# Performance work log

Hardware: AMD Instinct MI355X
Metric: run time of the kernel (lower is better)

Reference implementation:

```python
import jax, jax.numpy as jnp
import numpy as np

B, S, WIN5, E, H = 64, 2048, 50, 128, 256


def setup_inputs() -> dict:
    key = jax.random.key(0)
    ks = jax.random.split(key, 11)
    return {
        "prev_window": jax.random.normal(ks[0], (B, S, WIN5), dtype=jnp.float32),
        "W_emb": jax.random.normal(ks[1], (E, WIN5), dtype=jnp.float32) * 0.1,
        "b_emb": jax.random.normal(ks[2], (E,), dtype=jnp.float32) * 0.1,
        "W_ih": jax.random.normal(ks[3], (4 * H, E), dtype=jnp.float32) * 0.05,
        "W_hh": jax.random.normal(ks[4], (4 * H, H), dtype=jnp.float32) * 0.05,
        "b_ih": jax.random.normal(ks[5], (4 * H,), dtype=jnp.float32) * 0.05,
        "b_hh": jax.random.normal(ks[6], (4 * H,), dtype=jnp.float32) * 0.05,
        "W_out": jax.random.normal(ks[7], (1, H), dtype=jnp.float32) * 0.1,
        "b_out": jax.random.normal(ks[8], (1,), dtype=jnp.float32) * 0.1,
        "h0": jax.random.uniform(ks[9], (B, H), dtype=jnp.float32),
        "c0": jax.random.uniform(ks[10], (B, H), dtype=jnp.float32),
    }


def reference(prev_window, W_emb, b_emb, W_ih, W_hh, b_ih, b_hh, W_out, b_out, h0, c0):
    # embedding: [B, S, E], relu(Linear)
    emb = jax.nn.relu(jnp.einsum("bsw,ew->bse", prev_window, W_emb) + b_emb)
    # precompute input projections for all steps: [S, B, 4H]
    x_gates = jnp.einsum("bse,ge->sbg", emb, W_ih) + b_ih + b_hh

    def step(carry, xg):
        h, c = carry
        gates = xg + h @ W_hh.T  # [B, 4H]
        i, f, g, o = jnp.split(gates, 4, axis=-1)
        i = jax.nn.sigmoid(i)
        f = jax.nn.sigmoid(f)
        g = jnp.tanh(g)
        o = jax.nn.sigmoid(o)
        c = f * c + i * g
        h = o * jnp.tanh(c)
        return (h, c), h

    _, hs = jax.lax.scan(step, (h0, c0), x_gates)  # hs: [S, B, H]
    # dropout rate is 0.0 -> identity
    y = jax.nn.sigmoid(jnp.einsum("sbh,oh->sbo", hs, W_out) + b_out)  # [S, B, 1]
    return y
```

## Files before the change

### kernel.cpp

```cpp
#include <hip/hip_runtime.h>
#include <hip/hip_bf16.h>

#define B_ 64
#define S_ 2048
#define W_ 50
#define E_ 128
#define H_ 256
#define G_ 1024

typedef unsigned short u16;
typedef unsigned int u32;
typedef unsigned char u8;
typedef unsigned int v4u __attribute__((ext_vector_type(4)));
typedef __attribute__((ext_vector_type(8))) short short8;
typedef __attribute__((ext_vector_type(4))) float f32x4;

__device__ int g_mode;
__device__ u16 g_WA[E_ * G_];
__device__ float g_bias[G_];
__device__ u32 g_Wi8[G_ * 64];
__device__ float g_wscale[G_];
__device__ u16 g_xg[(size_t)B_ * S_ * G_];
__device__ float g_hs[(size_t)B_ * S_ * H_];

__device__ __forceinline__ float b2f(u16 u) {
    union { u32 i; float f; } v;
    v.i = ((u32)u) << 16;
    return v.f;
}
__device__ __forceinline__ u16 f2b(float f) {
    __hip_bfloat16 h = __float2bfloat16(f);
    return *reinterpret_cast<u16*>(&h);
}
__device__ __forceinline__ float ldin(int mode, const void* p, size_t i) {
    return mode ? ((const float*)p)[i] : b2f(((const u16*)p)[i]);
}
__device__ __forceinline__ float clamp30(float x) {
    return fminf(fmaxf(x, -30.0f), 30.0f);
}
__device__ __forceinline__ float sigmoidf_(float x) { return 1.0f / (1.0f + __expf(-x)); }
__device__ __forceinline__ float tanhf_(float x) {
    float e = __expf(2.0f * x);
    return 1.0f - 2.0f / (e + 1.0f);
}
__device__ __forceinline__ int dot4i8(u32 a, u32 b, int acc) {
#if __has_builtin(__builtin_amdgcn_sdot4)
    return __builtin_amdgcn_sdot4(a, b, acc, false);
#else
    acc += (int)(signed char)(a)       * (int)(signed char)(b);
    acc += (int)(signed char)(a >> 8)  * (int)(signed char)(b >> 8);
    acc += (int)(signed char)(a >> 16) * (int)(signed char)(b >> 16);
    acc += (int)(signed char)(a >> 24) * (int)(signed char)(b >> 24);
    return acc;
#endif
}

__global__ void sniff_kernel(const u16* __restrict__ wemb) {
    int sane = 0;
    for (int i = 0; i < 2048; ++i) {
        int ex = (wemb[i] >> 7) & 0xFF;
        if (ex == 0 || (ex >= 96 && ex <= 143)) ++sane;
    }
    g_mode = (sane >= 1900) ? 0 : 1;
}

__global__ __launch_bounds__(256) void prep_wa(const void* __restrict__ src) {
    const int mode = g_mode;
    int i = blockIdx.x * 256 + threadIdx.x;
    int j = i & 7, l = (i >> 3) & 63, ks = (i >> 9) & 3, ct = i >> 11;
    int c = ct * 16 + (l & 15);
    int e = ks * 32 + (l >> 4) * 8 + j;
    int row = ((c & 3) << 8) + (c >> 2);
    g_WA[i] = f2b(ldin(mode, src, (size_t)row * E_ + e));
}

__global__ __launch_bounds__(256) void prep_wi8(const void* __restrict__ src,
                                                const void* __restrict__ bih,
                                                const void* __restrict__ bhh) {
    const int mode = g_mode;
    int c = blockIdx.x * 256 + threadIdx.x;
    int row = ((c & 3) << 8) + (c >> 2);
    g_bias[c] = ldin(mode, bih, row) + ldin(mode, bhh, row);
    const size_t base = (size_t)row * H_;
    float m = 0.0f;
    for (int k = 0; k < H_; ++k) m = fmaxf(m, fabsf(ldin(mode, src, base + k)));
    float inv = (m > 0.0f) ? 127.0f / m : 0.0f;
    g_wscale[c] = m / (127.0f * 127.0f);
    for (int j = 0; j < 64; ++j) {
        u32 pk = 0;
#pragma unroll
        for (int i = 0; i < 4; ++i) {
            int q = (int)rintf(ldin(mode, src, base + 4 * j + i) * inv);
            q = max(-127, min(127, q));
            pk |= ((u32)(q & 0xff)) << (8 * i);
        }
        g_Wi8[(size_t)(c >> 2) * 256 + j * 4 + (c & 3)] = pk;
    }
}

__global__ __launch_bounds__(256) void xg_mfma(const void* __restrict__ pw,
                                               const void* __restrict__ Wemb,
                                               const void* __restrict__ bemb) {
    const int mode = g_mode;
    const int t = threadIdx.x;
    const int m0 = blockIdx.x * 16;
    __shared__ float pw16[16][W_ + 2];
    __shared__ float Wl[E_ * 51];
    __shared__ __align__(16) u16 embL[16][136];

    for (int i = t; i < E_ * W_; i += 256) {
        int e = i / W_, w = i - e * W_;
        Wl[e * 51 + w] = ldin(mode, Wemb, i);
    }
    for (int i = t; i < 16 * W_; i += 256) {
        int r = i / W_, w = i - r * W_;
        pw16[r][w] = ldin(mode, pw, (size_t)(m0 + r) * W_ + w);
    }
    __syncthreads();

#pragma unroll
    for (int i = 0; i < 8; ++i) {
        int idx = i * 256 + t;
        int r = idx >> 7, e = idx & 127;
        float a = ldin(mode, bemb, e);
        const float* wr = &Wl[e * 51];
#pragma unroll
        for (int w = 0; w < W_; ++w) a = fmaf(pw16[r][w], wr[w], a);
        embL[r][e] = f2b(fmaxf(a, 0.0f));
    }
    __syncthreads();

    const int l = t & 63;
    const int wv = t >> 6;
    short8 Bf0 = *(const short8*)&embL[l & 15][0 * 32 + (l >> 4) * 8];
    short8 Bf1 = *(const short8*)&embL[l & 15][1 * 32 + (l >> 4) * 8];
    short8 Bf2 = *(const short8*)&embL[l & 15][2 * 32 + (l >> 4) * 8];
    short8 Bf3 = *(const short8*)&embL[l & 15][3 * 32 + (l >> 4) * 8];
    const short8* wa = (const short8*)g_WA;
    const int m = m0 + (l & 15);
#pragma unroll
    for (int tt = 0; tt < 16; ++tt) {
        const int ct = wv * 16 + tt;
        const int cbase = ct * 16;
        const float4 bv = *(const float4*)(g_bias + cbase + 4 * (l >> 4));
        f32x4 acc = {bv.x, bv.y, bv.z, bv.w};
        acc = __builtin_amdgcn_mfma_f32_16x16x32_bf16(wa[(ct * 4 + 0) * 64 + l], Bf0, acc, 0, 0, 0);
        acc = __builtin_amdgcn_mfma_f32_16x16x32_bf16(wa[(ct * 4 + 1) * 64 + l], Bf1, acc, 0, 0, 0);
        acc = __builtin_amdgcn_mfma_f32_16x16x32_bf16(wa[(ct * 4 + 2) * 64 + l], Bf2, acc, 0, 0, 0);
        acc = __builtin_amdgcn_mfma_f32_16x16x32_bf16(wa[(ct * 4 + 3) * 64 + l], Bf3, acc, 0, 0, 0);
        u32 p0 = (u32)f2b(acc[0]) | ((u32)f2b(acc[1]) << 16);
        u32 p1 = (u32)f2b(acc[2]) | ((u32)f2b(acc[3]) << 16);
        uint2 pv; pv.x = p0; pv.y = p1;
        *(uint2*)(g_xg + (size_t)m * G_ + cbase + 4 * (l >> 4)) = pv;
    }
}

__global__ __launch_bounds__(512)
__attribute__((amdgpu_waves_per_eu(2, 2)))
void lstm_split(const void* __restrict__ h0, const void* __restrict__ c0) {
    const int mode = g_mode;
    const int t = threadIdx.x;
    const int b = blockIdx.x;
    const int u = t >> 1;
    const int half = t & 1;

    __shared__ __align__(16) u32 h8[2][H_ / 4];

    v4u W00, W01, W02, W03, W04, W05, W06, W07, W08, W09, W10, W11, W12, W13, W14, W15;
    v4u W16, W17, W18, W19, W20, W21, W22, W23, W24, W25, W26, W27, W28, W29, W30, W31;
    {
        const u32* wp = g_Wi8 + (size_t)t * 128;
        asm volatile(
            "global_load_dwordx4 %0, %16, off\n\t"
            "global_load_dwordx4 %1, %16, off offset:16\n\t"
            "global_load_dwordx4 %2, %16, off offset:32\n\t"
            "global_load_dwordx4 %3, %16, off offset:48\n\t"
            "global_load_dwordx4 %4, %16, off offset:64\n\t"
            "global_load_dwordx4 %5, %16, off offset:80\n\t"
            "global_load_dwordx4 %6, %16, off offset:96\n\t"
            "global_load_dwordx4 %7, %16, off offset:112\n\t"
            "global_load_dwordx4 %8, %16, off offset:128\n\t"
            "global_load_dwordx4 %9, %16, off offset:144\n\t"
            "global_load_dwordx4 %10, %16, off offset:160\n\t"
            "global_load_dwordx4 %11, %16, off offset:176\n\t"
            "global_load_dwordx4 %12, %16, off offset:192\n\t"
            "global_load_dwordx4 %13, %16, off offset:208\n\t"
            "global_load_dwordx4 %14, %16, off offset:224\n\t"
            "global_load_dwordx4 %15, %16, off offset:240\n\t"
            "s_waitcnt vmcnt(0)"
            : "=&v"(W00), "=&v"(W01), "=&v"(W02), "=&v"(W03),
              "=&v"(W04), "=&v"(W05), "=&v"(W06), "=&v"(W07),
              "=&v"(W08), "=&v"(W09), "=&v"(W10), "=&v"(W11),
              "=&v"(W12), "=&v"(W13), "=&v"(W14), "=&v"(W15)
            : "v"(wp));
        asm volatile(
            "global_load_dwordx4 %0, %16, off offset:256\n\t"
            "global_load_dwordx4 %1, %16, off offset:272\n\t"
            "global_load_dwordx4 %2, %16, off offset:288\n\t"
            "global_load_dwordx4 %3, %16, off offset:304\n\t"
            "global_load_dwordx4 %4, %16, off offset:320\n\t"
            "global_load_dwordx4 %5, %16, off offset:336\n\t"
            "global_load_dwordx4 %6, %16, off offset:352\n\t"
            "global_load_dwordx4 %7, %16, off offset:368\n\t"
            "global_load_dwordx4 %8, %16, off offset:384\n\t"
            "global_load_dwordx4 %9, %16, off offset:400\n\t"
            "global_load_dwordx4 %10, %16, off offset:416\n\t"
            "global_load_dwordx4 %11, %16, off offset:432\n\t"
            "global_load_dwordx4 %12, %16, off offset:448\n\t"
            "global_load_dwordx4 %13, %16, off offset:464\n\t"
            "global_load_dwordx4 %14, %16, off offset:480\n\t"
            "global_load_dwordx4 %15, %16, off offset:496\n\t"
            "s_waitcnt vmcnt(0)"
            : "=&v"(W16), "=&v"(W17), "=&v"(W18), "=&v"(W19),
              "=&v"(W20), "=&v"(W21), "=&v"(W22), "=&v"(W23),
              "=&v"(W24), "=&v"(W25), "=&v"(W26), "=&v"(W27),
              "=&v"(W28), "=&v"(W29), "=&v"(W30), "=&v"(W31)
            : "v"(wp));
    }

    const float4 wsc4 = *(const float4*)(g_wscale + 4 * u);
    float c_reg = (half == 0) ? ldin(mode, c0, (size_t)b * H_ + u) : 0.0f;

    if (t < H_ / 4) {
        u32 pk = 0;
#pragma unroll
        for (int i = 0; i < 4; ++i) {
            float h = ldin(mode, h0, (size_t)b * H_ + 4 * t + i);
            int q = (int)rintf(fminf(fmaxf(h, -1.0f), 1.0f) * 127.0f);
            pk |= ((u32)(q & 0xff)) << (8 * i);
        }
        h8[0][t] = pk;
    }
    const u16* xp = g_xg + (size_t)b * S_ * G_ + 4 * u;
    float* hsp = g_hs + (size_t)b * S_ * H_ + u;

    ushort4 xq[4];
#pragma unroll
    for (int e = 0; e < 4; ++e)
        xq[e] = *(const ushort4*)(xp + (size_t)e * G_);

    asm volatile("s_waitcnt lgkmcnt(0)\n\t"
                 "s_barrier" ::: "memory");

#define DOTG(HV, WA, WB, WC, WD)                                              \
            ai = dot4i8(HV.x, WA.x, ai); af = dot4i8(HV.x, WA.y, af);         \
            ag = dot4i8(HV.x, WA.z, ag); ao = dot4i8(HV.x, WA.w, ao);         \
            ai = dot4i8(HV.y, WB.x, ai); af = dot4i8(HV.y, WB.y, af);         \
            ag = dot4i8(HV.y, WB.z, ag); ao = dot4i8(HV.y, WB.w, ao);         \
            ai = dot4i8(HV.z, WC.x, ai); af = dot4i8(HV.z, WC.y, af);         \
            ag = dot4i8(HV.z, WC.z, ag); ao = dot4i8(HV.z, WC.w, ao);         \
            ai = dot4i8(HV.w, WD.x, ai); af = dot4i8(HV.w, WD.y, af);         \
            ag = dot4i8(HV.w, WD.z, ag); ao = dot4i8(HV.w, WD.w, ao);

    for (int s0 = 0; s0 < S_; s0 += 4) {
#pragma unroll
        for (int e = 0; e < 4; ++e) {
            const int s = s0 + e;
            const ushort4 xv = xq[e];
            const int sn = (s + 4 < S_) ? s + 4 : s;
            xq[e] = *(const ushort4*)(xp + (size_t)sn * G_);

            const uint4* hp = (const uint4*)h8[s & 1] + half * 8;
            uint4 h0v = hp[0], h1v = hp[1], h2v = hp[2], h3v = hp[3];
            uint4 h4v = hp[4], h5v = hp[5], h6v = hp[6], h7v = hp[7];

            int ai = 0, af = 0, ag = 0, ao = 0;
            DOTG(h0v, W00, W01, W02, W03)
            DOTG(h1v, W04, W05, W06, W07)
            DOTG(h2v, W08, W09, W10, W11)
            DOTG(h3v, W12, W13, W14, W15)
            DOTG(h4v, W16, W17, W18, W19)
            DOTG(h5v, W20, W21, W22, W23)
            DOTG(h6v, W24, W25, W26, W27)
            DOTG(h7v, W28, W29, W30, W31)

            ai += __shfl_xor(ai, 1, 64);
            af += __shfl_xor(af, 1, 64);
            ag += __shfl_xor(ag, 1, 64);
            ao += __shfl_xor(ao, 1, 64);

            if (half == 0) {
                float gi = (float)ai * wsc4.x + b2f(xv.x);
                float gf = (float)af * wsc4.y + b2f(xv.y);
                float gg = (float)ag * wsc4.z + b2f(xv.z);
                float go = (float)ao * wsc4.w + b2f(xv.w);
                float ii = sigmoidf_(clamp30(gi));
                float ff = sigmoidf_(clamp30(gf));
                float gv = tanhf_(clamp30(gg));
                float oo = sigmoidf_(clamp30(go));
                c_reg = fmaf(ff, c_reg, ii * gv);
                float h = oo * tanhf_(c_reg);
                int q = (int)rintf(fminf(fmaxf(h, -1.0f), 1.0f) * 127.0f) & 0xff;
                ((u8*)h8[(s + 1) & 1])[u] = (u8)q;
                hsp[(size_t)s * H_] = h;
            }
            asm volatile("s_waitcnt lgkmcnt(0)\n\t"
                         "s_barrier" ::: "memory");
        }
    }
#undef DOTG
}

__global__ __launch_bounds__(256) void head_kernel(const void* __restrict__ Wout,
                                                   const void* __restrict__ bout,
                                                   void* __restrict__ yv) {
    const int mode = g_mode;
    const int t = threadIdx.x;
    const int idx = blockIdx.x * 4 + (t >> 6);
    const int l = t & 63;
    const int s = idx >> 6, b = idx & 63;
    const float* hb = g_hs + ((size_t)b * S_ + s) * H_ + 4 * l;
    float4 hv = *(const float4*)hb;
    float p = hv.x * ldin(mode, Wout, 4 * l + 0)
            + hv.y * ldin(mode, Wout, 4 * l + 1)
            + hv.z * ldin(mode, Wout, 4 * l + 2)
            + hv.w * ldin(mode, Wout, 4 * l + 3);
#pragma unroll
    for (int off = 32; off > 0; off >>= 1) p += __shfl_down(p, off, 64);
    if (l == 0) {
        float yf = sigmoidf_(clamp30(p + ldin(mode, bout, 0)));
        if (mode) ((float*)yv)[(size_t)s * B_ + b] = yf;
        else      ((u16*)yv)[(size_t)s * B_ + b] = f2b(yf);
    }
}

extern "C" void kernel_launch(void* const* d_in, const int* in_sizes, int n_in,
                              void* d_out, int out_size, void* d_ws, size_t ws_size,
                              hipStream_t stream) {
    const void* pw   = d_in[0];
    const void* Wemb = d_in[1];
    const void* bemb = d_in[2];
    const void* Wih  = d_in[3];
    const void* Whh  = d_in[4];
    const void* bih  = d_in[5];
    const void* bhh  = d_in[6];
    const void* Wout = d_in[7];
    const void* bout = d_in[8];
    const void* h0   = d_in[9];
    const void* c0   = d_in[10];
    void* y = d_out;
    (void)d_ws; (void)ws_size;

    sniff_kernel<<<1, 1, 0, stream>>>((const u16*)Wemb);
    prep_wa<<<(E_ * G_) / 256, 256, 0, stream>>>(Wih);
    prep_wi8<<<G_ / 256, 256, 0, stream>>>(Whh, bih, bhh);
    xg_mfma<<<(B_ * S_) / 16, 256, 0, stream>>>(pw, Wemb, bemb);
    lstm_split<<<B_, 512, 0, stream>>>(h0, c0);
    head_kernel<<<(S_ * B_) / 4, 256, 0, stream>>>(Wout, bout, y);
}
```

Baseline: 2.575 ms.

## Compute LSTM recurrent matvec with int8 MFMA instead of sdot4

Replaces the per-thread sdot4 recurrent h·W_hh product with mfma_i32_16x16x32_i8 tiles. Each wave computes 128 gate rows against an h vector held in LDS, and a new prep kernel rearranges the int8 weights into MFMA A-operand layout. The gate accumulators are passed through a shared buffer to 32 lanes per wave, which then apply the nonlinearities. Only one of the 16 MFMA columns is useful, so most matrix compute is wasted, and each step adds an extra LDS round trip, trading VALU work for latency on the serial recurrence. The gate clamps are also removed.

```diff
diff --git a/kernel.cpp b/kernel.cpp
--- a/kernel.cpp
+++ b/kernel.cpp
@@ -14,11 +14,13 @@
 typedef unsigned int v4u __attribute__((ext_vector_type(4)));
 typedef __attribute__((ext_vector_type(8))) short short8;
 typedef __attribute__((ext_vector_type(4))) float f32x4;
+typedef __attribute__((ext_vector_type(4))) int i32x4;
 
 __device__ int g_mode;
 __device__ u16 g_WA[E_ * G_];
 __device__ float g_bias[G_];
 __device__ u32 g_Wi8[G_ * 64];
+__device__ u32 g_WqA[G_ * 64];
 __device__ float g_wscale[G_];
 __device__ u16 g_xg[(size_t)B_ * S_ * G_];
 __device__ float g_hs[(size_t)B_ * S_ * H_];
@@ -42,17 +44,6 @@
 __device__ __forceinline__ float tanhf_(float x) {
     float e = __expf(2.0f * x);
     return 1.0f - 2.0f / (e + 1.0f);
-}
-__device__ __forceinline__ int dot4i8(u32 a, u32 b, int acc) {
-#if __has_builtin(__builtin_amdgcn_sdot4)
-    return __builtin_amdgcn_sdot4(a, b, acc, false);
-#else
-    acc += (int)(signed char)(a)       * (int)(signed char)(b);
-    acc += (int)(signed char)(a >> 8)  * (int)(signed char)(b >> 8);
-    acc += (int)(signed char)(a >> 16) * (int)(signed char)(b >> 16);
-    acc += (int)(signed char)(a >> 24) * (int)(signed char)(b >> 24);
-    return acc;
-#endif
 }
 
 __global__ void sniff_kernel(const u16* __restrict__ wemb) {
@@ -96,6 +87,15 @@
         }
         g_Wi8[(size_t)(c >> 2) * 256 + j * 4 + (c & 3)] = pk;
     }
+}
+
+__global__ __launch_bounds__(256) void prep_wqa() {
+    int i = blockIdx.x * 256 + threadIdx.x;
+    int d = i & 1, r = i >> 1;
+    int kt = r & 7, mt = (r >> 3) & 7, l = (r >> 6) & 63, w = r >> 12;
+    int c = w * 128 + mt * 16 + (l & 15);
+    int k0 = kt * 32 + ((l >> 4) << 3) + d * 4;
+    g_WqA[i] = g_Wi8[(size_t)(c >> 2) * 256 + (k0 >> 2) * 4 + (c & 3)];
 }
 
 __global__ __launch_bounds__(256) void xg_mfma(const void* __restrict__ pw,
@@ -155,21 +155,30 @@
     }
 }
 
+#define MFMAI8(a, b, c) __builtin_amdgcn_mfma_i32_16x16x32_i8((a), (b), (c), 0, 0, 0)
+#define MKQ(lo, hi) ((long)((((unsigned long long)(hi)) << 32) | (lo)))
+#define MKL(v) ((long)((((unsigned long long)(v).y) << 32) | (v).x))
+
 __global__ __launch_bounds__(512)
 __attribute__((amdgpu_waves_per_eu(2, 2)))
-void lstm_split(const void* __restrict__ h0, const void* __restrict__ c0) {
+void lstm_mfma(const void* __restrict__ h0, const void* __restrict__ c0) {
     const int mode = g_mode;
     const int t = threadIdx.x;
     const int b = blockIdx.x;
-    const int u = t >> 1;
-    const int half = t & 1;
-
-    __shared__ __align__(16) u32 h8[2][H_ / 4];
-
-    v4u W00, W01, W02, W03, W04, W05, W06, W07, W08, W09, W10, W11, W12, W13, W14, W15;
-    v4u W16, W17, W18, W19, W20, W21, W22, W23, W24, W25, W26, W27, W28, W29, W30, W31;
+    const int w = t >> 6;
+    const int l = t & 63;
+    const int lg8 = (l >> 4) << 3;
+    const int lg4 = (l >> 4) << 2;
+    const bool lq0 = ((l & 15) == 0);
+    const int u = w * 32 + (l & 31);
+
+    __shared__ __align__(16) u32 h8[2][64];
+    __shared__ __align__(16) int gb[8][128];
+
+    v4u Q00, Q01, Q02, Q03, Q04, Q05, Q06, Q07, Q08, Q09, Q10, Q11, Q12, Q13, Q14, Q15;
+    v4u Q16, Q17, Q18, Q19, Q20, Q21, Q22, Q23, Q24, Q25, Q26, Q27, Q28, Q29, Q30, Q31;
     {
-        const u32* wp = g_Wi8 + (size_t)t * 128;
+        const u32* wp = g_WqA + (size_t)t * 128;
         asm volatile(
             "global_load_dwordx4 %0, %16, off\n\t"
             "global_load_dwordx4 %1, %16, off offset:16\n\t"
@@ -188,10 +197,10 @@
             "global_load_dwordx4 %14, %16, off offset:224\n\t"
             "global_load_dwordx4 %15, %16, off offset:240\n\t"
             "s_waitcnt vmcnt(0)"
-            : "=&v"(W00), "=&v"(W01), "=&v"(W02), "=&v"(W03),
-              "=&v"(W04), "=&v"(W05), "=&v"(W06), "=&v"(W07),
-              "=&v"(W08), "=&v"(W09), "=&v"(W10), "=&v"(W11),
-              "=&v"(W12), "=&v"(W13), "=&v"(W14), "=&v"(W15)
+            : "=&v"(Q00), "=&v"(Q01), "=&v"(Q02), "=&v"(Q03),
+              "=&v"(Q04), "=&v"(Q05), "=&v"(Q06), "=&v"(Q07),
+              "=&v"(Q08), "=&v"(Q09), "=&v"(Q10), "=&v"(Q11),
+              "=&v"(Q12), "=&v"(Q13), "=&v"(Q14), "=&v"(Q15)
             : "v"(wp));
         asm volatile(
             "global_load_dwordx4 %0, %16, off offset:256\n\t"
@@ -211,94 +220,96 @@
             "global_load_dwordx4 %14, %16, off offset:480\n\t"
             "global_load_dwordx4 %15, %16, off offset:496\n\t"
             "s_waitcnt vmcnt(0)"
-            : "=&v"(W16), "=&v"(W17), "=&v"(W18), "=&v"(W19),
-              "=&v"(W20), "=&v"(W21), "=&v"(W22), "=&v"(W23),
-              "=&v"(W24), "=&v"(W25), "=&v"(W26), "=&v"(W27),
-              "=&v"(W28), "=&v"(W29), "=&v"(W30), "=&v"(W31)
+            : "=&v"(Q16), "=&v"(Q17), "=&v"(Q18), "=&v"(Q19),
+              "=&v"(Q20), "=&v"(Q21), "=&v"(Q22), "=&v"(Q23),
+              "=&v"(Q24), "=&v"(Q25), "=&v"(Q26), "=&v"(Q27),
+              "=&v"(Q28), "=&v"(Q29), "=&v"(Q30), "=&v"(Q31)
             : "v"(wp));
     }
 
-    const float4 wsc4 = *(const float4*)(g_wscale + 4 * u);
-    float c_reg = (half == 0) ? ldin(mode, c0, (size_t)b * H_ + u) : 0.0f;
-
-    if (t < H_ / 4) {
-        u32 pk = 0;
-#pragma unroll
-        for (int i = 0; i < 4; ++i) {
-            float h = ldin(mode, h0, (size_t)b * H_ + 4 * t + i);
-            int q = (int)rintf(fminf(fmaxf(h, -1.0f), 1.0f) * 127.0f);
-            pk |= ((u32)(q & 0xff)) << (8 * i);
-        }
-        h8[0][t] = pk;
-    }
+    const float4 wsf4 = *(const float4*)(g_wscale + 4 * u);
     const u16* xp = g_xg + (size_t)b * S_ * G_ + 4 * u;
     float* hsp = g_hs + (size_t)b * S_ * H_ + u;
-
-    ushort4 xq[4];
-#pragma unroll
-    for (int e = 0; e < 4; ++e)
-        xq[e] = *(const ushort4*)(xp + (size_t)e * G_);
-
+    float c_reg = 0.0f;
+    ushort4 xqA, xqB;
+    xqA.x = xqA.y = xqA.z = xqA.w = 0;
+    xqB = xqA;
+    if (l < 32) {
+        c_reg = ldin(mode, c0, (size_t)b * H_ + u);
+        float hh = ldin(mode, h0, (size_t)b * H_ + u);
+        int q = (int)rintf(fminf(fmaxf(hh, -1.0f), 1.0f) * 127.0f) & 0xff;
+        ((u8*)&h8[0][0])[u] = (u8)q;
+        xqA = *(const ushort4*)(xp);
+        xqB = *(const ushort4*)(xp + G_);
+    }
     asm volatile("s_waitcnt lgkmcnt(0)\n\t"
                  "s_barrier" ::: "memory");
 
-#define DOTG(HV, WA, WB, WC, WD)                                              \
-            ai = dot4i8(HV.x, WA.x, ai); af = dot4i8(HV.x, WA.y, af);         \
-            ag = dot4i8(HV.x, WA.z, ag); ao = dot4i8(HV.x, WA.w, ao);         \
-            ai = dot4i8(HV.y, WB.x, ai); af = dot4i8(HV.y, WB.y, af);         \
-            ag = dot4i8(HV.y, WB.z, ag); ao = dot4i8(HV.y, WB.w, ao);         \
-            ai = dot4i8(HV.z, WC.x, ai); af = dot4i8(HV.z, WC.y, af);         \
-            ag = dot4i8(HV.z, WC.z, ag); ao = dot4i8(HV.z, WC.w, ao);         \
-            ai = dot4i8(HV.w, WD.x, ai); af = dot4i8(HV.w, WD.y, af);         \
-            ag = dot4i8(HV.w, WD.z, ag); ao = dot4i8(HV.w, WD.w, ao);
-
-    for (int s0 = 0; s0 < S_; s0 += 4) {
-#pragma unroll
-        for (int e = 0; e < 4; ++e) {
-            const int s = s0 + e;
-            const ushort4 xv = xq[e];
-            const int sn = (s + 4 < S_) ? s + 4 : s;
-            xq[e] = *(const ushort4*)(xp + (size_t)sn * G_);
-
-            const uint4* hp = (const uint4*)h8[s & 1] + half * 8;
-            uint4 h0v = hp[0], h1v = hp[1], h2v = hp[2], h3v = hp[3];
-            uint4 h4v = hp[4], h5v = hp[5], h6v = hp[6], h7v = hp[7];
-
-            int ai = 0, af = 0, ag = 0, ao = 0;
-            DOTG(h0v, W00, W01, W02, W03)
-            DOTG(h1v, W04, W05, W06, W07)
-            DOTG(h2v, W08, W09, W10, W11)
-            DOTG(h3v, W12, W13, W14, W15)
-            DOTG(h4v, W16, W17, W18, W19)
-            DOTG(h5v, W20, W21, W22, W23)
-            DOTG(h6v, W24, W25, W26, W27)
-            DOTG(h7v, W28, W29, W30, W31)
-
-            ai += __shfl_xor(ai, 1, 64);
-            af += __shfl_xor(af, 1, 64);
-            ag += __shfl_xor(ag, 1, 64);
-            ao += __shfl_xor(ao, 1, 64);
-
-            if (half == 0) {
-                float gi = (float)ai * wsc4.x + b2f(xv.x);
-                float gf = (float)af * wsc4.y + b2f(xv.y);
-                float gg = (float)ag * wsc4.z + b2f(xv.z);
-                float go = (float)ao * wsc4.w + b2f(xv.w);
-                float ii = sigmoidf_(clamp30(gi));
-                float ff = sigmoidf_(clamp30(gf));
-                float gv = tanhf_(clamp30(gg));
-                float oo = sigmoidf_(clamp30(go));
-                c_reg = fmaf(ff, c_reg, ii * gv);
-                float h = oo * tanhf_(c_reg);
-                int q = (int)rintf(fminf(fmaxf(h, -1.0f), 1.0f) * 127.0f) & 0xff;
-                ((u8*)h8[(s + 1) & 1])[u] = (u8)q;
-                hsp[(size_t)s * H_] = h;
-            }
-            asm volatile("s_waitcnt lgkmcnt(0)\n\t"
-                         "s_barrier" ::: "memory");
-        }
-    }
-#undef DOTG
+#define MTROW(mt, QA, QB, QC, QD, B0, B1, B2, B3, B4, B5, B6, B7)             \
+    {                                                                         \
+        i32x4 acc = {0, 0, 0, 0};                                             \
+        acc = MFMAI8(MKQ(QA.x, QA.y), B0, acc);                               \
+        acc = MFMAI8(MKQ(QA.z, QA.w), B1, acc);                               \
+        acc = MFMAI8(MKQ(QB.x, QB.y), B2, acc);                               \
+        acc = MFMAI8(MKQ(QB.z, QB.w), B3, acc);                               \
+        acc = MFMAI8(MKQ(QC.x, QC.y), B4, acc);                               \
+        acc = MFMAI8(MKQ(QC.z, QC.w), B5, acc);                               \
+        acc = MFMAI8(MKQ(QD.x, QD.y), B6, acc);                               \
+        acc = MFMAI8(MKQ(QD.z, QD.w), B7, acc);                               \
+        if (lq0) *(i32x4*)&gb[w][(mt) * 16 + lg4] = acc;                      \
+    }
+
+#define STEP(S, XQ, SN)                                                       \
+    {                                                                         \
+        const u8* hb = (const u8*)&h8[(S) & 1][0];                            \
+        uint2 bf0 = *(const uint2*)(hb + 0 * 32 + lg8);                       \
+        uint2 bf1 = *(const uint2*)(hb + 1 * 32 + lg8);                       \
+        uint2 bf2 = *(const uint2*)(hb + 2 * 32 + lg8);                       \
+        uint2 bf3 = *(const uint2*)(hb + 3 * 32 + lg8);                       \
+        uint2 bf4 = *(const uint2*)(hb + 4 * 32 + lg8);                       \
+        uint2 bf5 = *(const uint2*)(hb + 5 * 32 + lg8);                       \
+        uint2 bf6 = *(const uint2*)(hb + 6 * 32 + lg8);                       \
+        uint2 bf7 = *(const uint2*)(hb + 7 * 32 + lg8);                       \
+        const long Bl0 = MKL(bf0), Bl1 = MKL(bf1), Bl2 = MKL(bf2);            \
+        const long Bl3 = MKL(bf3), Bl4 = MKL(bf4), Bl5 = MKL(bf5);            \
+        const long Bl6 = MKL(bf6), Bl7 = MKL(bf7);                            \
+        MTROW(0, Q00, Q01, Q02, Q03, Bl0, Bl1, Bl2, Bl3, Bl4, Bl5, Bl6, Bl7)  \
+        MTROW(1, Q04, Q05, Q06, Q07, Bl0, Bl1, Bl2, Bl3, Bl4, Bl5, Bl6, Bl7)  \
+        MTROW(2, Q08, Q09, Q10, Q11, Bl0, Bl1, Bl2, Bl3, Bl4, Bl5, Bl6, Bl7)  \
+        MTROW(3, Q12, Q13, Q14, Q15, Bl0, Bl1, Bl2, Bl3, Bl4, Bl5, Bl6, Bl7)  \
+        MTROW(4, Q16, Q17, Q18, Q19, Bl0, Bl1, Bl2, Bl3, Bl4, Bl5, Bl6, Bl7)  \
+        MTROW(5, Q20, Q21, Q22, Q23, Bl0, Bl1, Bl2, Bl3, Bl4, Bl5, Bl6, Bl7)  \
+        MTROW(6, Q24, Q25, Q26, Q27, Bl0, Bl1, Bl2, Bl3, Bl4, Bl5, Bl6, Bl7)  \
+        MTROW(7, Q28, Q29, Q30, Q31, Bl0, Bl1, Bl2, Bl3, Bl4, Bl5, Bl6, Bl7)  \
+        asm volatile("s_waitcnt lgkmcnt(0)" ::: "memory");                    \
+        if (l < 32) {                                                         \
+            const i32x4 gv = *(const i32x4*)&gb[w][4 * (l & 31)];             \
+            const ushort4 xv = XQ;                                            \
+            XQ = *(const ushort4*)(xp + (size_t)(SN) * G_);                   \
+            float gi = (float)gv.x * wsf4.x + b2f(xv.x);                      \
+            float gf = (float)gv.y * wsf4.y + b2f(xv.y);                      \
+            float gg = (float)gv.z * wsf4.z + b2f(xv.z);                      \
+            float go = (float)gv.w * wsf4.w + b2f(xv.w);                      \
+            float ii = sigmoidf_(gi);                                         \
+            float ff = sigmoidf_(gf);                                         \
+            float gt = tanhf_(gg);                                            \
+            float oo = sigmoidf_(go);                                         \
+            c_reg = fmaf(ff, c_reg, ii * gt);                                 \
+            float hv = oo * tanhf_(c_reg);                                    \
+            ((u8*)&h8[((S) + 1) & 1][0])[u] =                                 \
+                (u8)((int)rintf(hv * 127.0f) & 0xff);                         \
+            hsp[(size_t)(S) * H_] = hv;                                       \
+        }                                                                     \
+        asm volatile("s_waitcnt lgkmcnt(0)\n\t"                               \
+                     "s_barrier" ::: "memory");                               \
+    }
+
+    for (int s0 = 0; s0 < S_; s0 += 2) {
+        STEP(s0,     xqA, (s0 + 2 < S_) ? s0 + 2 : s0)
+        STEP(s0 + 1, xqB, (s0 + 3 < S_) ? s0 + 3 : s0 + 1)
+    }
+#undef STEP
+#undef MTROW
 }
 
 __global__ __launch_bounds__(256) void head_kernel(const void* __restrict__ Wout,
@@ -344,7 +355,8 @@
     sniff_kernel<<<1, 1, 0, stream>>>((const u16*)Wemb);
     prep_wa<<<(E_ * G_) / 256, 256, 0, stream>>>(Wih);
     prep_wi8<<<G_ / 256, 256, 0, stream>>>(Whh, bih, bhh);
+    prep_wqa<<<(G_ * 64) / 256, 256, 0, stream>>>();
     xg_mfma<<<(B_ * S_) / 16, 256, 0, stream>>>(pw, Wemb, bemb);
-    lstm_split<<<B_, 512, 0, stream>>>(h0, c0);
+    lstm_mfma<<<B_, 512, 0, stream>>>(h0, c0);
     head_kernel<<<(S_ * B_) / 4, 256, 0, stream>>>(Wout, bout, y);
 }
```

Result: slower. 3.980 ms (+54.5%).
